# Kernel tuning notes

Hardware: AMD Instinct MI355X
Metric: run time of the kernel (lower is better)

Reference implementation:

```python
import jax, jax.numpy as jnp
import numpy as np

_A = -0.75  # PyTorch bicubic coefficient

def _c1(u):
    return ((_A + 2) * u - (_A + 3)) * u * u + 1

def _c2(u):
    return ((_A * u - 5 * _A) * u + 8 * _A) * u - 4 * _A

def bicubic_up(x, out_len):
    # 1D bicubic along last axis, matching torch Upsample(mode='bicubic',
    # align_corners=False) on a [*, L, 1] tensor (width dim is identity).
    L = x.shape[-1]
    scale = L / out_len
    src = (jnp.arange(out_len, dtype=jnp.float32) + 0.5) * scale - 0.5
    i0 = jnp.floor(src)
    t = src - i0
    w = jnp.stack([_c2(t + 1), _c1(t), _c1(1 - t), _c2(2 - t)], axis=-1)  # [out,4]
    idx = jnp.clip(i0.astype(jnp.int32)[:, None] + jnp.arange(-1, 3), 0, L - 1)  # [out,4]
    return jnp.sum(x[..., idx] * w.astype(x.dtype), axis=-1)

def bn(x, g, b, eps=1e-5):
    # BatchNorm1d in training mode: batch stats over (batch, length) per channel
    m = jnp.mean(x, axis=(0, 2), keepdims=True)
    v = jnp.mean((x - m) ** 2, axis=(0, 2), keepdims=True)
    return (x - m) * jax.lax.rsqrt(v + eps) * g[None, :, None] + b[None, :, None]

def lrelu(x):
    return jnp.where(x >= 0, x, 0.2 * x)

def setup_inputs() -> dict:
    key = jax.random.key(0)
    ks = jax.random.split(key, 16)
    B = 4096
    d = {
        'x': jax.random.normal(ks[0], (B, 1, 160), jnp.float32),
        'y': jax.random.randint(ks[1], (B,), 0, 3, jnp.int32),
        'emb': jax.random.normal(ks[2], (3, 50), jnp.float32),
        'Wc': jax.random.normal(ks[3], (117, 50), jnp.float32) * (1 / np.sqrt(50)),
        'bc': jnp.zeros((117,), jnp.float32),
        'Wi': jax.random.normal(ks[4], (936, 160), jnp.float32) * (1 / np.sqrt(160)),
        'bi': jnp.zeros((936,), jnp.float32),
        'g0': jax.random.normal(ks[5], (1,), jnp.float32) * 0.02,
        'b0': jnp.zeros((1,), jnp.float32),
        'w1': jax.random.normal(ks[6], (8, 9), jnp.float32) * 0.02,
        'w2': jax.random.normal(ks[7], (8, 8), jnp.float32) * 0.02,
        'w3': jax.random.normal(ks[8], (8, 8), jnp.float32) * 0.02,
        'w4': jax.random.normal(ks[9], (8, 8), jnp.float32) * 0.02,
        'w5': jax.random.normal(ks[10], (8, 8), jnp.float32) * 0.02,
        'w6': jax.random.normal(ks[11], (1, 8), jnp.float32) * 0.02,
    }
    for i in range(1, 6):
        d[f'g{i}'] = jax.random.normal(ks[11 + i], (8,), jnp.float32) * 0.02
        d[f'b{i}'] = jnp.zeros((8,), jnp.float32)
    return d

def reference(x, y, emb, Wc, bc, Wi, bi, g0, b0,
              w1, w2, w3, w4, w5, w6,
              g1, b1, g2, b2, g3, b3, g4, b4, g5, b5):
    B = x.shape[0]
    # class branch: Embedding -> Linear -> [B,1,117]
    oc = (emb[y] @ Wc.T + bc).reshape(B, 1, 117)
    # input branch: Linear -> BatchNorm1d(1) -> LeakyReLU -> [B,8,117]
    oi = jnp.einsum('bil,ol->bio', x, Wi) + bi  # [B,1,936]
    oi = lrelu(bn(oi, g0, b0)).reshape(B, 8, 117)
    out = jnp.concatenate([oi, oc], axis=1)  # [B,9,117]
    stages = [(234, w1, g1, b1), (468, w2, g2, b2), (937, w3, g3, b3),
              (1875, w4, g4, b4), (3750, w5, g5, b5)]
    for out_len, w, g, b in stages:
        out = bicubic_up(out, out_len)
        out = jnp.einsum('oc,bcl->bol', w, out)  # 1x1 conv (no bias)
        out = lrelu(bn(out, g, b))
    out = jnp.einsum('oc,bcl->bol', w6, out)  # [B,1,3750]
    return out
```

## Files before the change

### kernel.cpp

```cpp
#include <hip/hip_runtime.h>
#include <math.h>

#define BATCH 4096
#define L0 117
#define L1 234
#define L2 468
#define L3 937
#define L4 1875
#define L5 3750
#define JC 512
#define NTAB (L1 + L2 + L3 + L4 + L5)
#define NBT  (L0 + L1 + L2 + L3 + L4)
#define NSTATS (16 + 5 * 64 * 16)

static __device__ __forceinline__ float lrelu(float v) { return v >= 0.f ? v : 0.2f * v; }

__global__ void k_setup(double* __restrict__ stats, int* __restrict__ ti0,
                        float4* __restrict__ tw)
{
    int s = blockIdx.x;
    if (s == 0)
        for (int i = threadIdx.x; i < NSTATS; i += blockDim.x) stats[i] = 0.0;
    const int Lin[5]  = {L0, L1, L2, L3, L4};
    const int Lout[5] = {L1, L2, L3, L4, L5};
    const int Uoff[5] = {0, L1, L1 + L2, L1 + L2 + L3, L1 + L2 + L3 + L4};
    int li = Lin[s], lo = Lout[s], off = Uoff[s];
    float scale = (float)((double)li / (double)lo);
    const float A = -0.75f;
    for (int j = threadIdx.x; j < lo; j += blockDim.x) {
        float src = ((float)j + 0.5f) * scale - 0.5f;
        float fi = floorf(src);
        float t = src - fi;
        float u;
        float4 w;
        u = t + 1.f; w.x = ((A * u - 5.f * A) * u + 8.f * A) * u - 4.f * A;
        u = t;       w.y = ((A + 2.f) * u - (A + 3.f)) * u * u + 1.f;
        u = 1.f - t; w.z = ((A + 2.f) * u - (A + 3.f)) * u * u + 1.f;
        u = 2.f - t; w.w = ((A * u - 5.f * A) * u + 8.f * A) * u - 4.f * A;
        ti0[off + j] = (int)fi;
        tw[off + j] = w;
    }
}

__global__ __launch_bounds__(256) void k_setup2(float* __restrict__ colsum,
                                                float4* __restrict__ band)
{
    __shared__ float cs[1880];
    __shared__ float bd[1880][4];
    int s = blockIdx.x;
    const int Lin[5]  = {L0, L1, L2, L3, L4};
    const int Lout[5] = {L1, L2, L3, L4, L5};
    const int Toff[5] = {0, L0, L0 + L1, L0 + L1 + L2, L0 + L1 + L2 + L3};
    int li = Lin[s], lo = Lout[s], off = Toff[s];
    for (int i = threadIdx.x; i < li; i += 256) {
        cs[i] = 0.f; bd[i][0] = 0.f; bd[i][1] = 0.f; bd[i][2] = 0.f; bd[i][3] = 0.f;
    }
    __syncthreads();
    float scale = (float)((double)li / (double)lo);
    const float A = -0.75f;
    for (int j = threadIdx.x; j < lo; j += 256) {
        float src = ((float)j + 0.5f) * scale - 0.5f;
        float fi = floorf(src);
        float t = src - fi;
        int i0 = (int)fi;
        float u, w[4];
        u = t + 1.f; w[0] = ((A * u - 5.f * A) * u + 8.f * A) * u - 4.f * A;
        u = t;       w[1] = ((A + 2.f) * u - (A + 3.f)) * u * u + 1.f;
        u = 1.f - t; w[2] = ((A + 2.f) * u - (A + 3.f)) * u * u + 1.f;
        u = 2.f - t; w[3] = ((A * u - 5.f * A) * u + 8.f * A) * u - 4.f * A;
        int q[4];
#pragma unroll
        for (int k = 0; k < 4; k++) q[k] = min(max(i0 - 1 + k, 0), li - 1);
#pragma unroll
        for (int k = 0; k < 4; k++) atomicAdd(&cs[q[k]], w[k]);
#pragma unroll
        for (int k = 0; k < 4; k++)
#pragma unroll
            for (int l = 0; l < 4; l++) {
                int qa = q[k], qb = q[l];
                int qm = min(qa, qb), d = abs(qa - qb);
                atomicAdd(&bd[qm][d], w[k] * w[l]);
            }
    }
    __syncthreads();
    for (int i = threadIdx.x; i < li; i += 256) {
        colsum[off + i] = cs[i];
        band[off + i] = make_float4(bd[i][0], bd[i][1], bd[i][2], bd[i][3]);
    }
}

__global__ void k_coef(const double* __restrict__ zb, const float* __restrict__ g,
                       const float* __restrict__ bb, double N,
                       float* __restrict__ coef)
{
    __shared__ double col[16];
    int tid = threadIdx.x;
    if (tid < 16) {
        double s = 0.0;
        for (int k = 0; k < 64; k++) s += zb[k * 16 + tid];
        col[tid] = s;
    }
    __syncthreads();
    if (tid < 8) {
        double m = col[tid] / N;
        double var = col[8 + tid] / N - m * m;
        double a = (double)g[tid] / sqrt(var + 1e-5);
        coef[tid] = (float)a;
        coef[8 + tid] = (float)((double)bb[tid] - m * a);
    }
}

__global__ __launch_bounds__(256) void k0a(const float* __restrict__ x,
                                           const float* __restrict__ Wi,
                                           const float* __restrict__ bi,
                                           float* __restrict__ oi,
                                           double* __restrict__ stats)
{
    __shared__ float As[32][68];
    __shared__ float Bs[32][132];
    __shared__ float red[512];
    int m0 = blockIdx.y * 64;
    int n0 = blockIdx.x * 128;
    int tid = threadIdx.x;
    int tm = tid >> 4, tn = tid & 15;
    float acc[4][8];
#pragma unroll
    for (int r = 0; r < 4; r++)
#pragma unroll
        for (int c = 0; c < 8; c++) acc[r][c] = 0.f;

    for (int k0 = 0; k0 < 160; k0 += 32) {
        for (int e = tid; e < 64 * 32; e += 256) {
            int m = e >> 5, k = e & 31;
            As[k][m] = x[(size_t)(m0 + m) * 160 + k0 + k];
        }
        for (int e = tid; e < 128 * 32; e += 256) {
            int n = e >> 5, k = e & 31;
            int row = n0 + n;
            Bs[k][n] = (row < 936) ? Wi[(size_t)row * 160 + k0 + k] : 0.f;
        }
        __syncthreads();
#pragma unroll
        for (int k = 0; k < 32; k++) {
            float4 av = *(const float4*)&As[k][tm * 4];
            float4 bv0 = *(const float4*)&Bs[k][tn * 8];
            float4 bv1 = *(const float4*)&Bs[k][tn * 8 + 4];
            float a[4] = {av.x, av.y, av.z, av.w};
            float b[8] = {bv0.x, bv0.y, bv0.z, bv0.w, bv1.x, bv1.y, bv1.z, bv1.w};
#pragma unroll
            for (int r = 0; r < 4; r++)
#pragma unroll
                for (int c = 0; c < 8; c++) acc[r][c] = fmaf(a[r], b[c], acc[r][c]);
        }
        __syncthreads();
    }
    float lsum = 0.f, lsq = 0.f;
#pragma unroll
    for (int r = 0; r < 4; r++) {
        int row = m0 + tm * 4 + r;
        int col = n0 + tn * 8;
        float vals[8];
#pragma unroll
        for (int c = 0; c < 8; c++) {
            float v = (col + c < 936) ? acc[r][c] + bi[col + c] : 0.f;
            vals[c] = v;
            lsum += v;
            lsq += v * v;
        }
        if (col + 7 < 936) {
            *(float4*)&oi[(size_t)row * 936 + col] = make_float4(vals[0], vals[1], vals[2], vals[3]);
            *(float4*)&oi[(size_t)row * 936 + col + 4] = make_float4(vals[4], vals[5], vals[6], vals[7]);
        } else {
            for (int c = 0; c < 8; c++)
                if (col + c < 936) oi[(size_t)row * 936 + col + c] = vals[c];
        }
    }
    red[tid] = lsum;
    red[256 + tid] = lsq;
    __syncthreads();
    for (int st = 128; st > 0; st >>= 1) {
        if (tid < st) { red[tid] += red[tid + st]; red[256 + tid] += red[256 + tid + st]; }
        __syncthreads();
    }
    if (tid == 0) {
        atomicAdd(&stats[0], (double)red[0]);
        atomicAdd(&stats[1], (double)red[256]);
    }
}

__global__ __launch_bounds__(128) void k0b(const float* __restrict__ oi,
                                           const float* __restrict__ emb,
                                           const int* __restrict__ y,
                                           const float* __restrict__ Wc,
                                           const float* __restrict__ bc,
                                           const float* __restrict__ g0,
                                           const float* __restrict__ b0,
                                           const float* __restrict__ w1,
                                           const double* __restrict__ st0,
                                           double* __restrict__ z1out,
                                           const float* __restrict__ colsum1,
                                           const float4* __restrict__ band1,
                                           float* __restrict__ v1)
{
    __shared__ float embs[50], W1s[72];
    __shared__ float sa_s, sc_s;
    __shared__ float vs[117][9];
    __shared__ float red[2][16];
    int b = blockIdx.x, tid = threadIdx.x;
    if (tid < 50) embs[tid] = emb[y[b] * 50 + tid];
    else if (tid < 122) W1s[tid - 50] = w1[tid - 50];
    else if (tid == 122) {
        double N = (double)BATCH * 936.0;
        double m = st0[0] / N;
        double var = st0[1] / N - m * m;
        double a = (double)g0[0] / sqrt(var + 1e-5);
        sa_s = (float)a;
        sc_s = (float)((double)b0[0] - m * a);
    }
    __syncthreads();
    float ls[8], lq[8];
#pragma unroll
    for (int o = 0; o < 8; o++) { ls[o] = 0.f; lq[o] = 0.f; }
    if (tid < 117) {
        float oc = bc[tid];
        for (int k = 0; k < 50; k++) oc = fmaf(embs[k], Wc[tid * 50 + k], oc);
        float h[9];
#pragma unroll
        for (int c = 0; c < 8; c++)
            h[c] = lrelu(fmaf(oi[(size_t)b * 936 + c * 117 + tid], sa_s, sc_s));
        h[8] = oc;
        float vn[8];
#pragma unroll
        for (int o = 0; o < 8; o++) {
            float a2 = 0.f;
#pragma unroll
            for (int c = 0; c < 9; c++) a2 = fmaf(W1s[o * 9 + c], h[c], a2);
            vn[o] = a2;
        }
        float* dp = v1 + ((size_t)b * 117 + tid) * 8;
        *(float4*)dp = make_float4(vn[0], vn[1], vn[2], vn[3]);
        *(float4*)(dp + 4) = make_float4(vn[4], vn[5], vn[6], vn[7]);
#pragma unroll
        for (int o = 0; o < 8; o++) vs[tid][o] = vn[o];
    }
    __syncthreads();
    if (tid < 117) {
        float csv = colsum1[tid];
        float4 bdv = band1[tid];
#pragma unroll
        for (int o = 0; o < 8; o++) {
            float v0 = vs[tid][o];
            ls[o] = fmaf(csv, v0, ls[o]);
            float t = bdv.x * v0;
            if (tid + 1 < 117) t = fmaf(bdv.y, vs[tid + 1][o], t);
            if (tid + 2 < 117) t = fmaf(bdv.z, vs[tid + 2][o], t);
            if (tid + 3 < 117) t = fmaf(bdv.w, vs[tid + 3][o], t);
            lq[o] = fmaf(v0, t, lq[o]);
        }
    }
#pragma unroll
    for (int o = 0; o < 8; o++)
        for (int off = 32; off > 0; off >>= 1) {
            ls[o] += __shfl_down(ls[o], off, 64);
            lq[o] += __shfl_down(lq[o], off, 64);
        }
    int wave = tid >> 6, lane = tid & 63;
    if (lane == 0)
#pragma unroll
        for (int o = 0; o < 8; o++) { red[wave][o] = ls[o]; red[wave][8 + o] = lq[o]; }
    __syncthreads();
    if (tid < 16)
        atomicAdd(&z1out[(b & 63) * 16 + tid], (double)(red[0][tid] + red[1][tid]));
}

template <int LIN, int LOUT>
__global__ __launch_bounds__(256, 2) void k_stage(
    const float* __restrict__ vin, float* __restrict__ vout,
    const float* __restrict__ W, const float* __restrict__ coef,
    double* __restrict__ zout,
    const float* __restrict__ colsum, const float4* __restrict__ band,
    const int* __restrict__ ti0, const float4* __restrict__ tw)
{
    constexpr int NCH = (LOUT + JC - 1) / JC;
    constexpr int VSN = (LOUT < JC ? LOUT : JC) + 3;
    __shared__ float Ws[64], aa[8], cc[8];
    __shared__ float vins[LIN][9];
    __shared__ float vs[VSN][9];
    __shared__ float red[4][16];
    int tid = threadIdx.x;
    if (tid < 64) Ws[tid] = W[tid];
    if (tid < 8) { aa[tid] = coef[tid]; cc[tid] = coef[8 + tid]; }
    int b = blockIdx.x;
    const float4* srcp = (const float4*)(vin + (size_t)b * LIN * 8);
    for (int f = tid; f < LIN * 2; f += 256) {
        float4 v = srcp[f];
        int q = f >> 1, hf = (f & 1) * 4;
        vins[q][hf + 0] = v.x; vins[q][hf + 1] = v.y;
        vins[q][hf + 2] = v.z; vins[q][hf + 3] = v.w;
    }
    float ls[8], lq[8];
#pragma unroll
    for (int o = 0; o < 8; o++) { ls[o] = 0.f; lq[o] = 0.f; }
    __syncthreads();

    for (int ch = 0; ch < NCH; ch++) {
        int j0 = ch * JC, j1 = min(j0 + JC, LOUT), je = min(j1 + 3, LOUT);
        for (int jj = tid; jj < je - j0; jj += 256) {
            int j = j0 + jj;
            int i0 = ti0[j];
            float4 w = tw[j];
            float wk[4] = {w.x, w.y, w.z, w.w};
            float z[8] = {0.f, 0.f, 0.f, 0.f, 0.f, 0.f, 0.f, 0.f};
#pragma unroll
            for (int k = 0; k < 4; k++) {
                int q = min(max(i0 - 1 + k, 0), LIN - 1);
                const float* vp = vins[q];
#pragma unroll
                for (int c = 0; c < 8; c++) z[c] = fmaf(wk[k], vp[c], z[c]);
            }
            float h[8];
#pragma unroll
            for (int c = 0; c < 8; c++) h[c] = lrelu(fmaf(z[c], aa[c], cc[c]));
            float vn[8];
#pragma unroll
            for (int o = 0; o < 8; o++) {
                float a2 = 0.f;
#pragma unroll
                for (int c = 0; c < 8; c++) a2 = fmaf(Ws[o * 8 + c], h[c], a2);
                vn[o] = a2;
            }
            if (vout != nullptr && jj < j1 - j0) {
                float* dp = vout + ((size_t)b * LOUT + j) * 8;
                *(float4*)dp = make_float4(vn[0], vn[1], vn[2], vn[3]);
                *(float4*)(dp + 4) = make_float4(vn[4], vn[5], vn[6], vn[7]);
            }
#pragma unroll
            for (int o = 0; o < 8; o++) vs[jj][o] = vn[o];
        }
        __syncthreads();
        int nst = j1 - j0, ne = je - j0;
        for (int jj = tid; jj < nst; jj += 256) {
            int p = j0 + jj;
            float csv = colsum[p];
            float4 bdv = band[p];
#pragma unroll
            for (int o = 0; o < 8; o++) {
                float v0 = vs[jj][o];
                ls[o] = fmaf(csv, v0, ls[o]);
                float t = bdv.x * v0;
                if (jj + 1 < ne) t = fmaf(bdv.y, vs[jj + 1][o], t);
                if (jj + 2 < ne) t = fmaf(bdv.z, vs[jj + 2][o], t);
                if (jj + 3 < ne) t = fmaf(bdv.w, vs[jj + 3][o], t);
                lq[o] = fmaf(v0, t, lq[o]);
            }
        }
        __syncthreads();
    }

#pragma unroll
    for (int o = 0; o < 8; o++)
        for (int off = 32; off > 0; off >>= 1) {
            ls[o] += __shfl_down(ls[o], off, 64);
            lq[o] += __shfl_down(lq[o], off, 64);
        }
    int wave = tid >> 6, lane = tid & 63;
    if (lane == 0)
#pragma unroll
        for (int o = 0; o < 8; o++) { red[wave][o] = ls[o]; red[wave][8 + o] = lq[o]; }
    __syncthreads();
    if (tid < 16) {
        float v = red[0][tid] + red[1][tid] + red[2][tid] + red[3][tid];
        atomicAdd(&zout[(blockIdx.x & 63) * 16 + tid], (double)v);
    }
}

__global__ __launch_bounds__(256, 2) void k_final(
    const float* __restrict__ v4, float* __restrict__ out,
    const float* __restrict__ W5, const float* __restrict__ w6,
    const float* __restrict__ coef4, const float* __restrict__ coef5,
    const int* __restrict__ ti04, const float4* __restrict__ tw4,
    const int* __restrict__ ti05, const float4* __restrict__ tw5)
{
    __shared__ float W5s[64], w6s[8], a4[8], c4[8], a5[8], c5[8];
    __shared__ float v4s[L3][9];
    __shared__ float v5s[264][9];
    int tid = threadIdx.x;
    if (tid < 64) W5s[tid] = W5[tid];
    if (tid < 8) {
        w6s[tid] = w6[tid];
        a4[tid] = coef4[tid]; c4[tid] = coef4[8 + tid];
        a5[tid] = coef5[tid]; c5[tid] = coef5[8 + tid];
    }
    int b = blockIdx.x;
    const float4* srcp = (const float4*)(v4 + (size_t)b * L3 * 8);
    for (int f = tid; f < L3 * 2; f += 256) {
        float4 v = srcp[f];
        int q = f >> 1, hf = (f & 1) * 4;
        v4s[q][hf + 0] = v.x; v4s[q][hf + 1] = v.y;
        v4s[q][hf + 2] = v.z; v4s[q][hf + 3] = v.w;
    }
    __syncthreads();

    for (int ch = 0; ch < 8; ch++) {
        int j0 = ch * JC, j1 = min(j0 + JC, L5);
        int plo = max(0, ti05[j0] - 1);
        int phi = min(L4 - 1, ti05[j1 - 1] + 2);
        int NP = phi - plo + 1;
        for (int pp = tid; pp < NP; pp += 256) {
            int p = plo + pp;
            int i0 = ti04[p];
            float4 w = tw4[p];
            float wk[4] = {w.x, w.y, w.z, w.w};
            float z[8] = {0.f, 0.f, 0.f, 0.f, 0.f, 0.f, 0.f, 0.f};
#pragma unroll
            for (int k = 0; k < 4; k++) {
                int q = min(max(i0 - 1 + k, 0), L3 - 1);
                const float* vp = v4s[q];
#pragma unroll
                for (int c = 0; c < 8; c++) z[c] = fmaf(wk[k], vp[c], z[c]);
            }
            float h[8];
#pragma unroll
            for (int c = 0; c < 8; c++) h[c] = lrelu(fmaf(z[c], a4[c], c4[c]));
#pragma unroll
            for (int o = 0; o < 8; o++) {
                float a2 = 0.f;
#pragma unroll
                for (int c = 0; c < 8; c++) a2 = fmaf(W5s[o * 8 + c], h[c], a2);
                v5s[pp][o] = a2;
            }
        }
        __syncthreads();
        for (int jj = tid; jj < j1 - j0; jj += 256) {
            int j = j0 + jj;
            int i0 = ti05[j];
            float4 w = tw5[j];
            float wk[4] = {w.x, w.y, w.z, w.w};
            float z[8] = {0.f, 0.f, 0.f, 0.f, 0.f, 0.f, 0.f, 0.f};
#pragma unroll
            for (int k = 0; k < 4; k++) {
                int pp = min(max(i0 - 1 + k, 0), L4 - 1) - plo;
                const float* vp = v5s[pp];
#pragma unroll
                for (int o = 0; o < 8; o++) z[o] = fmaf(wk[k], vp[o], z[o]);
            }
            float r = 0.f;
#pragma unroll
            for (int o = 0; o < 8; o++)
                r = fmaf(w6s[o], lrelu(fmaf(z[o], a5[o], c5[o])), r);
            out[(size_t)b * L5 + j] = r;
        }
        __syncthreads();
    }
}

extern "C" void kernel_launch(void* const* d_in, const int* in_sizes, int n_in,
                              void* d_out, int out_size, void* d_ws, size_t ws_size,
                              hipStream_t stream)
{
    const float* x   = (const float*)d_in[0];
    const int*   y   = (const int*)d_in[1];
    const float* emb = (const float*)d_in[2];
    const float* Wc  = (const float*)d_in[3];
    const float* bc  = (const float*)d_in[4];
    const float* Wi  = (const float*)d_in[5];
    const float* bi  = (const float*)d_in[6];
    const float* g0  = (const float*)d_in[7];
    const float* b0  = (const float*)d_in[8];
    const float* w1  = (const float*)d_in[9];
    const float* w2  = (const float*)d_in[10];
    const float* w3  = (const float*)d_in[11];
    const float* w4  = (const float*)d_in[12];
    const float* w5  = (const float*)d_in[13];
    const float* w6  = (const float*)d_in[14];
    const float* g1  = (const float*)d_in[15];
    const float* b1  = (const float*)d_in[16];
    const float* g2  = (const float*)d_in[17];
    const float* b2  = (const float*)d_in[18];
    const float* g3  = (const float*)d_in[19];
    const float* b3  = (const float*)d_in[20];
    const float* g4  = (const float*)d_in[21];
    const float* b4  = (const float*)d_in[22];
    const float* g5  = (const float*)d_in[23];
    const float* b5  = (const float*)d_in[24];
    float* out = (float*)d_out;

    char* ws = (char*)d_ws;
    size_t off = 0;
    auto alloc = [&](size_t bytes) {
        size_t r = off;
        off += (bytes + 255) & ~(size_t)255;
        return r;
    };
    double* stats  = (double*)(ws + alloc(NSTATS * sizeof(double)));
    float*  coefs  = (float*)(ws + alloc(5 * 16 * sizeof(float)));
    int*    ti0    = (int*)(ws + alloc((size_t)NTAB * sizeof(int)));
    float4* tw     = (float4*)(ws + alloc((size_t)NTAB * sizeof(float4)));
    float*  colsum = (float*)(ws + alloc((size_t)NBT * sizeof(float)));
    float4* band   = (float4*)(ws + alloc((size_t)NBT * sizeof(float4)));
    float*  oi     = (float*)(ws + alloc((size_t)BATCH * 936 * 4));
    float*  bufA   = (float*)(ws + alloc((size_t)BATCH * L2 * 8 * 4));
    float*  bufB   = (float*)(ws + alloc((size_t)BATCH * L3 * 8 * 4));

    double* st0  = stats;
    double* zst1 = stats + 16;
    double* zst2 = stats + 16 + 1024;
    double* zst3 = stats + 16 + 2048;
    double* zst4 = stats + 16 + 3072;
    double* zst5 = stats + 16 + 4096;
    float* coef1 = coefs +  0;
    float* coef2 = coefs + 16;
    float* coef3 = coefs + 32;
    float* coef4 = coefs + 48;
    float* coef5 = coefs + 64;

    const int u1 = 0, u2 = L1, u3 = L1 + L2, u4 = L1 + L2 + L3, u5 = L1 + L2 + L3 + L4;
    const int t1 = 0, t2 = L0, t3 = L0 + L1, t4 = L0 + L1 + L2, t5 = L0 + L1 + L2 + L3;

    float* v1 = bufA;
    float* v2 = bufB;
    float* v3 = bufA;
    float* v4 = bufB;

    k_setup<<<5, 256, 0, stream>>>(stats, ti0, tw);
    k_setup2<<<5, 256, 0, stream>>>(colsum, band);
    k0a<<<dim3(8, 64), 256, 0, stream>>>(x, Wi, bi, oi, st0);
    k0b<<<BATCH, 128, 0, stream>>>(oi, emb, y, Wc, bc, g0, b0, w1, st0, zst1,
                                   colsum + t1, band + t1, v1);
    k_coef<<<1, 64, 0, stream>>>(zst1, g1, b1, (double)BATCH * L1, coef1);
    k_stage<L0, L1><<<BATCH, 256, 0, stream>>>(v1, v2, w2, coef1, zst2,
                                               colsum + t2, band + t2, ti0 + u1, tw + u1);
    k_coef<<<1, 64, 0, stream>>>(zst2, g2, b2, (double)BATCH * L2, coef2);
    k_stage<L1, L2><<<BATCH, 256, 0, stream>>>(v2, v3, w3, coef2, zst3,
                                               colsum + t3, band + t3, ti0 + u2, tw + u2);
    k_coef<<<1, 64, 0, stream>>>(zst3, g3, b3, (double)BATCH * L3, coef3);
    k_stage<L2, L3><<<BATCH, 256, 0, stream>>>(v3, v4, w4, coef3, zst4,
                                               colsum + t4, band + t4, ti0 + u3, tw + u3);
    k_coef<<<1, 64, 0, stream>>>(zst4, g4, b4, (double)BATCH * L4, coef4);
    k_stage<L3, L4><<<BATCH, 256, 0, stream>>>(v4, nullptr, w5, coef4, zst5,
                                               colsum + t5, band + t5, ti0 + u4, tw + u4);
    k_coef<<<1, 64, 0, stream>>>(zst5, g5, b5, (double)BATCH * L5, coef5);
    k_final<<<BATCH, 256, 0, stream>>>(v4, out, w5, w6, coef4, coef5,
                                       ti0 + u4, tw + u4, ti0 + u5, tw + u5);
}
```

Measured before the change: 858.2 us.

## Give each wave its own output chunk and compute bicubic weights inline

```diff
diff --git a/kernel.cpp b/kernel.cpp
--- a/kernel.cpp
+++ b/kernel.cpp
@@ -8,38 +8,28 @@
 #define L3 937
 #define L4 1875
 #define L5 3750
-#define JC 512
-#define NTAB (L1 + L2 + L3 + L4 + L5)
 #define NBT  (L0 + L1 + L2 + L3 + L4)
 #define NSTATS (16 + 5 * 64 * 16)
 
 static __device__ __forceinline__ float lrelu(float v) { return v >= 0.f ? v : 0.2f * v; }
 
-__global__ void k_setup(double* __restrict__ stats, int* __restrict__ ti0,
-                        float4* __restrict__ tw)
-{
-    int s = blockIdx.x;
-    if (s == 0)
-        for (int i = threadIdx.x; i < NSTATS; i += blockDim.x) stats[i] = 0.0;
-    const int Lin[5]  = {L0, L1, L2, L3, L4};
-    const int Lout[5] = {L1, L2, L3, L4, L5};
-    const int Uoff[5] = {0, L1, L1 + L2, L1 + L2 + L3, L1 + L2 + L3 + L4};
-    int li = Lin[s], lo = Lout[s], off = Uoff[s];
-    float scale = (float)((double)li / (double)lo);
+static __device__ __forceinline__ void bicw(int j, float scale, int& i0, float* w)
+{
+    float src = ((float)j + 0.5f) * scale - 0.5f;
+    float fi = floorf(src);
+    float t = src - fi;
     const float A = -0.75f;
-    for (int j = threadIdx.x; j < lo; j += blockDim.x) {
-        float src = ((float)j + 0.5f) * scale - 0.5f;
-        float fi = floorf(src);
-        float t = src - fi;
-        float u;
-        float4 w;
-        u = t + 1.f; w.x = ((A * u - 5.f * A) * u + 8.f * A) * u - 4.f * A;
-        u = t;       w.y = ((A + 2.f) * u - (A + 3.f)) * u * u + 1.f;
-        u = 1.f - t; w.z = ((A + 2.f) * u - (A + 3.f)) * u * u + 1.f;
-        u = 2.f - t; w.w = ((A * u - 5.f * A) * u + 8.f * A) * u - 4.f * A;
-        ti0[off + j] = (int)fi;
-        tw[off + j] = w;
-    }
+    float u;
+    u = t + 1.f; w[0] = ((A * u - 5.f * A) * u + 8.f * A) * u - 4.f * A;
+    u = t;       w[1] = ((A + 2.f) * u - (A + 3.f)) * u * u + 1.f;
+    u = 1.f - t; w[2] = ((A + 2.f) * u - (A + 3.f)) * u * u + 1.f;
+    u = 2.f - t; w[3] = ((A * u - 5.f * A) * u + 8.f * A) * u - 4.f * A;
+    i0 = (int)fi;
+}
+
+__global__ void k_setup(double* __restrict__ stats)
+{
+    for (int i = threadIdx.x; i < NSTATS; i += blockDim.x) stats[i] = 0.0;
 }
 
 __global__ __launch_bounds__(256) void k_setup2(float* __restrict__ colsum,
@@ -57,17 +47,10 @@
     }
     __syncthreads();
     float scale = (float)((double)li / (double)lo);
-    const float A = -0.75f;
     for (int j = threadIdx.x; j < lo; j += 256) {
-        float src = ((float)j + 0.5f) * scale - 0.5f;
-        float fi = floorf(src);
-        float t = src - fi;
-        int i0 = (int)fi;
-        float u, w[4];
-        u = t + 1.f; w[0] = ((A * u - 5.f * A) * u + 8.f * A) * u - 4.f * A;
-        u = t;       w[1] = ((A + 2.f) * u - (A + 3.f)) * u * u + 1.f;
-        u = 1.f - t; w[2] = ((A + 2.f) * u - (A + 3.f)) * u * u + 1.f;
-        u = 2.f - t; w[3] = ((A * u - 5.f * A) * u + 8.f * A) * u - 4.f * A;
+        int i0;
+        float w[4];
+        bicw(j, scale, i0, w);
         int q[4];
 #pragma unroll
         for (int k = 0; k < 4; k++) q[k] = min(max(i0 - 1 + k, 0), li - 1);
@@ -278,16 +261,15 @@
     const float* __restrict__ vin, float* __restrict__ vout,
     const float* __restrict__ W, const float* __restrict__ coef,
     double* __restrict__ zout,
-    const float* __restrict__ colsum, const float4* __restrict__ band,
-    const int* __restrict__ ti0, const float4* __restrict__ tw)
-{
-    constexpr int NCH = (LOUT + JC - 1) / JC;
-    constexpr int VSN = (LOUT < JC ? LOUT : JC) + 3;
+    const float* __restrict__ colsum, const float4* __restrict__ band)
+{
+    constexpr int JCW = (LOUT + 7) / 8;
     __shared__ float Ws[64], aa[8], cc[8];
     __shared__ float vins[LIN][9];
-    __shared__ float vs[VSN][9];
+    __shared__ float vs[4][JCW + 3][9];
     __shared__ float red[4][16];
     int tid = threadIdx.x;
+    int wave = tid >> 6, lane = tid & 63;
     if (tid < 64) Ws[tid] = W[tid];
     if (tid < 8) { aa[tid] = coef[tid]; cc[tid] = coef[8 + tid]; }
     int b = blockIdx.x;
@@ -301,15 +283,19 @@
     float ls[8], lq[8];
 #pragma unroll
     for (int o = 0; o < 8; o++) { ls[o] = 0.f; lq[o] = 0.f; }
-    __syncthreads();
-
-    for (int ch = 0; ch < NCH; ch++) {
-        int j0 = ch * JC, j1 = min(j0 + JC, LOUT), je = min(j1 + 3, LOUT);
-        for (int jj = tid; jj < je - j0; jj += 256) {
+    const float scale = (float)((double)LIN / (double)LOUT);
+    __syncthreads();
+
+    float (*vsw)[9] = vs[wave];
+    for (int ch = wave; ch < 8; ch += 4) {
+        int j0 = ch * JCW, j1 = min(j0 + JCW, LOUT);
+        if (j0 >= LOUT) break;
+        int je = min(j1 + 3, LOUT);
+        for (int jj = lane; jj < je - j0; jj += 64) {
             int j = j0 + jj;
-            int i0 = ti0[j];
-            float4 w = tw[j];
-            float wk[4] = {w.x, w.y, w.z, w.w};
+            int i0;
+            float wk[4];
+            bicw(j, scale, i0, wk);
             float z[8] = {0.f, 0.f, 0.f, 0.f, 0.f, 0.f, 0.f, 0.f};
 #pragma unroll
             for (int k = 0; k < 4; k++) {
@@ -335,26 +321,26 @@
                 *(float4*)(dp + 4) = make_float4(vn[4], vn[5], vn[6], vn[7]);
             }
 #pragma unroll
-            for (int o = 0; o < 8; o++) vs[jj][o] = vn[o];
-        }
-        __syncthreads();
+            for (int o = 0; o < 8; o++) vsw[jj][o] = vn[o];
+        }
+        asm volatile("s_waitcnt lgkmcnt(0)" ::: "memory");
         int nst = j1 - j0, ne = je - j0;
-        for (int jj = tid; jj < nst; jj += 256) {
+        for (int jj = lane; jj < nst; jj += 64) {
             int p = j0 + jj;
             float csv = colsum[p];
             float4 bdv = band[p];
 #pragma unroll
             for (int o = 0; o < 8; o++) {
-                float v0 = vs[jj][o];
+                float v0 = vsw[jj][o];
                 ls[o] = fmaf(csv, v0, ls[o]);
                 float t = bdv.x * v0;
-                if (jj + 1 < ne) t = fmaf(bdv.y, vs[jj + 1][o], t);
-                if (jj + 2 < ne) t = fmaf(bdv.z, vs[jj + 2][o], t);
-                if (jj + 3 < ne) t = fmaf(bdv.w, vs[jj + 3][o], t);
+                if (jj + 1 < ne) t = fmaf(bdv.y, vsw[jj + 1][o], t);
+                if (jj + 2 < ne) t = fmaf(bdv.z, vsw[jj + 2][o], t);
+                if (jj + 3 < ne) t = fmaf(bdv.w, vsw[jj + 3][o], t);
                 lq[o] = fmaf(v0, t, lq[o]);
             }
         }
-        __syncthreads();
+        asm volatile("s_waitcnt lgkmcnt(0)" ::: "memory");
     }
 
 #pragma unroll
@@ -363,7 +349,6 @@
             ls[o] += __shfl_down(ls[o], off, 64);
             lq[o] += __shfl_down(lq[o], off, 64);
         }
-    int wave = tid >> 6, lane = tid & 63;
     if (lane == 0)
 #pragma unroll
         for (int o = 0; o < 8; o++) { red[wave][o] = ls[o]; red[wave][8 + o] = lq[o]; }
@@ -377,14 +362,14 @@
 __global__ __launch_bounds__(256, 2) void k_final(
     const float* __restrict__ v4, float* __restrict__ out,
     const float* __restrict__ W5, const float* __restrict__ w6,
-    const float* __restrict__ coef4, const float* __restrict__ coef5,
-    const int* __restrict__ ti04, const float4* __restrict__ tw4,
-    const int* __restrict__ ti05, const float4* __restrict__ tw5)
-{
+    const float* __restrict__ coef4, const float* __restrict__ coef5)
+{
+    constexpr int JCW = (L5 + 7) / 8;
     __shared__ float W5s[64], w6s[8], a4[8], c4[8], a5[8], c5[8];
     __shared__ float v4s[L3][9];
-    __shared__ float v5s[264][9];
+    __shared__ float v5s[4][242][9];
     int tid = threadIdx.x;
+    int wave = tid >> 6, lane = tid & 63;
     if (tid < 64) W5s[tid] = W5[tid];
     if (tid < 8) {
         w6s[tid] = w6[tid];
@@ -399,18 +384,26 @@
         v4s[q][hf + 0] = v.x; v4s[q][hf + 1] = v.y;
         v4s[q][hf + 2] = v.z; v4s[q][hf + 3] = v.w;
     }
-    __syncthreads();
-
-    for (int ch = 0; ch < 8; ch++) {
-        int j0 = ch * JC, j1 = min(j0 + JC, L5);
-        int plo = max(0, ti05[j0] - 1);
-        int phi = min(L4 - 1, ti05[j1 - 1] + 2);
+    const float scale4 = (float)((double)L3 / (double)L4);
+    const float scale5 = (float)((double)L4 / (double)L5);
+    __syncthreads();
+
+    float (*v5w)[9] = v5s[wave];
+    for (int ch = wave; ch < 8; ch += 4) {
+        int j0 = ch * JCW, j1 = min(j0 + JCW, L5);
+        if (j0 >= L5) break;
+        int i0a, i0b;
+        float wt[4];
+        bicw(j0, scale5, i0a, wt);
+        bicw(j1 - 1, scale5, i0b, wt);
+        int plo = max(0, i0a - 1);
+        int phi = min(L4 - 1, i0b + 2);
         int NP = phi - plo + 1;
-        for (int pp = tid; pp < NP; pp += 256) {
+        for (int pp = lane; pp < NP; pp += 64) {
             int p = plo + pp;
-            int i0 = ti04[p];
-            float4 w = tw4[p];
-            float wk[4] = {w.x, w.y, w.z, w.w};
+            int i0;
+            float wk[4];
+            bicw(p, scale4, i0, wk);
             float z[8] = {0.f, 0.f, 0.f, 0.f, 0.f, 0.f, 0.f, 0.f};
 #pragma unroll
             for (int k = 0; k < 4; k++) {
@@ -427,20 +420,20 @@
                 float a2 = 0.f;
 #pragma unroll
                 for (int c = 0; c < 8; c++) a2 = fmaf(W5s[o * 8 + c], h[c], a2);
-                v5s[pp][o] = a2;
-            }
-        }
-        __syncthreads();
-        for (int jj = tid; jj < j1 - j0; jj += 256) {
+                v5w[pp][o] = a2;
+            }
+        }
+        asm volatile("s_waitcnt lgkmcnt(0)" ::: "memory");
+        for (int jj = lane; jj < j1 - j0; jj += 64) {
             int j = j0 + jj;
-            int i0 = ti05[j];
-            float4 w = tw5[j];
-            float wk[4] = {w.x, w.y, w.z, w.w};
+            int i0;
+            float wk[4];
+            bicw(j, scale5, i0, wk);
             float z[8] = {0.f, 0.f, 0.f, 0.f, 0.f, 0.f, 0.f, 0.f};
 #pragma unroll
             for (int k = 0; k < 4; k++) {
                 int pp = min(max(i0 - 1 + k, 0), L4 - 1) - plo;
-                const float* vp = v5s[pp];
+                const float* vp = v5w[pp];
 #pragma unroll
                 for (int o = 0; o < 8; o++) z[o] = fmaf(wk[k], vp[o], z[o]);
             }
@@ -450,7 +443,7 @@
                 r = fmaf(w6s[o], lrelu(fmaf(z[o], a5[o], c5[o])), r);
             out[(size_t)b * L5 + j] = r;
         }
-        __syncthreads();
+        asm volatile("s_waitcnt lgkmcnt(0)" ::: "memory");
     }
 }
 
@@ -494,8 +487,6 @@
     };
     double* stats  = (double*)(ws + alloc(NSTATS * sizeof(double)));
     float*  coefs  = (float*)(ws + alloc(5 * 16 * sizeof(float)));
-    int*    ti0    = (int*)(ws + alloc((size_t)NTAB * sizeof(int)));
-    float4* tw     = (float4*)(ws + alloc((size_t)NTAB * sizeof(float4)));
     float*  colsum = (float*)(ws + alloc((size_t)NBT * sizeof(float)));
     float4* band   = (float4*)(ws + alloc((size_t)NBT * sizeof(float4)));
     float*  oi     = (float*)(ws + alloc((size_t)BATCH * 936 * 4));
@@ -514,7 +505,6 @@
     float* coef4 = coefs + 48;
     float* coef5 = coefs + 64;
 
-    const int u1 = 0, u2 = L1, u3 = L1 + L2, u4 = L1 + L2 + L3, u5 = L1 + L2 + L3 + L4;
     const int t1 = 0, t2 = L0, t3 = L0 + L1, t4 = L0 + L1 + L2, t5 = L0 + L1 + L2 + L3;
 
     float* v1 = bufA;
@@ -522,24 +512,23 @@
     float* v3 = bufA;
     float* v4 = bufB;
 
-    k_setup<<<5, 256, 0, stream>>>(stats, ti0, tw);
+    k_setup<<<1, 256, 0, stream>>>(stats);
     k_setup2<<<5, 256, 0, stream>>>(colsum, band);
     k0a<<<dim3(8, 64), 256, 0, stream>>>(x, Wi, bi, oi, st0);
     k0b<<<BATCH, 128, 0, stream>>>(oi, emb, y, Wc, bc, g0, b0, w1, st0, zst1,
                                    colsum + t1, band + t1, v1);
     k_coef<<<1, 64, 0, stream>>>(zst1, g1, b1, (double)BATCH * L1, coef1);
     k_stage<L0, L1><<<BATCH, 256, 0, stream>>>(v1, v2, w2, coef1, zst2,
-                                               colsum + t2, band + t2, ti0 + u1, tw + u1);
+                                               colsum + t2, band + t2);
     k_coef<<<1, 64, 0, stream>>>(zst2, g2, b2, (double)BATCH * L2, coef2);
     k_stage<L1, L2><<<BATCH, 256, 0, stream>>>(v2, v3, w3, coef2, zst3,
-                                               colsum + t3, band + t3, ti0 + u2, tw + u2);
+                                               colsum + t3, band + t3);
     k_coef<<<1, 64, 0, stream>>>(zst3, g3, b3, (double)BATCH * L3, coef3);
     k_stage<L2, L3><<<BATCH, 256, 0, stream>>>(v3, v4, w4, coef3, zst4,
-                                               colsum + t4, band + t4, ti0 + u3, tw + u3);
+                                               colsum + t4, band + t4);
     k_coef<<<1, 64, 0, stream>>>(zst4, g4, b4, (double)BATCH * L4, coef4);
     k_stage<L3, L4><<<BATCH, 256, 0, stream>>>(v4, nullptr, w5, coef4, zst5,
-                                               colsum + t5, band + t5, ti0 + u4, tw + u4);
+                                               colsum + t5, band + t5);
     k_coef<<<1, 64, 0, stream>>>(zst5, g5, b5, (double)BATCH * L5, coef5);
-    k_final<<<BATCH, 256, 0, stream>>>(v4, out, w5, w6, coef4, coef5,
-                                       ti0 + u4, tw + u4, ti0 + u5, tw + u5);
-}
+    k_final<<<BATCH, 256, 0, stream>>>(v4, out, w5, w6, coef4, coef5);
+}
```

Measured after the change: 818.9 us. -4.6%, faster.
